# Kernel tuning notes

Hardware: AMD Instinct MI355X
Metric: run time of the kernel (lower is better)

## Reference

```python
import jax, jax.numpy as jnp
import numpy as np
from jax.scipy.special import gammaln

B, N, K = 16, 65536, 64


def setup_inputs() -> dict:
    key = jax.random.key(0)
    k1, k2, k3, k4, k5 = jax.random.split(key, 5)
    x = jax.random.normal(k1, (B, N), dtype=jnp.float32)
    loc = jnp.full((1,), 0.5, dtype=jnp.float32)          # mean of Normal alpha prior
    scale = jnp.full((1,), -2.0, dtype=jnp.float32)       # softplus(-2) ~ 0.127
    epsilon = jax.random.normal(k3, (1,), dtype=jnp.float32)
    lags = jax.random.randint(k4, (K,), 1, N - 1, dtype=jnp.int64)
    return {"x": x, "loc": loc, "scale": scale, "epsilon": epsilon, "lags": lags}


def _stochastic_frac_deriv(x, alpha, lags):
    """Monte-Carlo Marchaud fractional derivative with k sampled memory lags.

    D^a f(t) ~ a/Gamma(1-a) * (N-1)/k * sum_m (f(t) - f(t - j_m)) * j_m^{-a-1}
    with the term masked out when t < j_m (history does not exist).
    """
    n = x.shape[-1]
    k = lags.shape[0]
    j = jnp.clip(lags, 1, n - 1)                      # [k]
    t = jnp.arange(n)                                 # [N]
    idx = jnp.maximum(t[None, :] - j[:, None], 0)     # [k, N]
    mask = (t[None, :] >= j[:, None]).astype(x.dtype) # [k, N]
    w = j.astype(x.dtype) ** (-(alpha + 1.0))         # kernel weight s^{-a-1}, [k]
    c = alpha * jnp.exp(-gammaln(1.0 - alpha)) * (n - 1) / k  # normalization * MC volume
    xg = x[:, idx]                                    # [B, k, N] gathered history
    contrib = (x[:, None, :] - xg) * (mask * w[:, None])[None, :, :]
    return c * contrib.sum(axis=1)                    # [B, N]


def reference(x, loc, scale, epsilon, lags):
    # reparameterized alpha ~ Normal(loc, softplus(scale))
    alpha = (loc + jax.nn.softplus(scale) * epsilon)[0]
    alpha = jnp.clip(alpha, 0.01, 0.99)               # keep fractional order valid
    return _stochastic_frac_deriv(x, alpha, lags)
```

## Files before the change

kernel.cpp:

```cpp
#include <hip/hip_runtime.h>

#define BB 16
#define NN 65536
#define KK 64
#define TPB 256
#define CHUNK 512
#define NBLK ((BB * NN) / CHUNK)

__device__ __forceinline__ float readlane_f(float v, int lane) {
    return __uint_as_float((unsigned)__builtin_amdgcn_readlane((int)__float_as_uint(v), lane));
}

__global__ __launch_bounds__(TPB) void frac_deriv_kernel(
    const float* __restrict__ x,
    const float* __restrict__ loc,
    const float* __restrict__ scale,
    const float* __restrict__ eps,
    const int* __restrict__ lags,
    float* __restrict__ out)
{
    __shared__ int   js_raw[KK];
    __shared__ float ws_raw[KK];
    __shared__ int   js[KK];
    __shared__ float ws[KK];
    __shared__ int   cnt[2];

    const int tid = threadIdx.x;
    const int bid = blockIdx.x;
    const int swz = (bid & 7) * (NBLK / 8) + (bid >> 3);
    const int b   = swz >> 7;
    const int q   = swz & 127;
    const int T   = q * CHUNK;

    if (tid < KK) {
        double s  = (double)scale[0];
        double sp = (s > 20.0) ? s : log1p(exp(s));
        double a  = (double)loc[0] + sp * (double)eps[0];
        a = fmin(fmax(a, 0.01), 0.99);
        double c = a * exp(-lgamma(1.0 - a)) * ((double)(NN - 1) / (double)KK);
        int j = lags[tid];
        j = (j < 1) ? 1 : ((j > NN - 1) ? NN - 1 : j);
        js_raw[tid] = j;
        ws_raw[tid] = (float)(c * exp(-(a + 1.0) * log((double)j)));
    }
    __syncthreads();
    if (tid < KK) {
        const int j = js_raw[tid];
        int rank = 0;
        for (int k = 0; k < KK; ++k) {
            const int jk = js_raw[k];
            rank += (int)((jk < j) || (jk == j && k < tid));
        }
        js[rank] = j;
        ws[rank] = ws_raw[tid];
    }
    __syncthreads();
    if (tid < 64) {
        const int j = js[tid];
        const unsigned long long mf = __ballot(j <= T);
        const unsigned long long mp = __ballot(j <= T + (CHUNK - 1));
        if (tid == 0) { cnt[0] = __popcll(mf); cnt[1] = __popcll(mp); }
    }
    __syncthreads();

    const int   jv = js[tid & 63];
    const float wv = ws[tid & 63];

    const float* __restrict__ xr = x + (size_t)b * NN;
    const float xt0 = xr[T + tid];
    const float xt1 = xr[T + 256 + tid];

    double acc0 = 0.0, acc1 = 0.0;

    const int cf  = __builtin_amdgcn_readfirstlane(cnt[0]);
    const int cp  = __builtin_amdgcn_readfirstlane(cnt[1]);
    const int cf8 = cf & ~7;

    for (int mo = 0; mo < cf8; mo += 8) {
        float g0 = 0.0f, g1 = 0.0f;
#pragma unroll
        for (int mi = 0; mi < 8; ++mi) {
            const int   m  = mo + mi;
            const int   jj = __builtin_amdgcn_readlane(jv, m);
            const float w  = readlane_f(wv, m);
            const float* bp = xr + (T - jj);
            const float x0 = bp[tid];
            const float x1 = bp[tid + 256];
            g0 = fmaf(xt0 - x0, w, g0);
            g1 = fmaf(xt1 - x1, w, g1);
        }
        acc0 += (double)g0;
        acc1 += (double)g1;
    }
    for (int m = cf8; m < cf; ++m) {
        const int   jj = __builtin_amdgcn_readlane(jv, m);
        const float w  = readlane_f(wv, m);
        const float* bp = xr + (T - jj);
        acc0 += (double)((xt0 - bp[tid]) * w);
        acc1 += (double)((xt1 - bp[tid + 256]) * w);
    }
    for (int m = cf; m < cp; ++m) {
        const int   jj = __builtin_amdgcn_readlane(jv, m);
        const float w  = readlane_f(wv, m);
        const int d0 = T + tid - jj;
        const int d1 = d0 + 256;
        const float g0v = xr[(d0 < 0) ? 0 : d0];
        const float g1v = xr[(d1 < 0) ? 0 : d1];
        acc0 += (d0 >= 0) ? (double)((xt0 - g0v) * w) : 0.0;
        acc1 += (d1 >= 0) ? (double)((xt1 - g1v) * w) : 0.0;
    }

    float* __restrict__ orow = out + (size_t)b * NN;
    orow[T + tid]       = (float)acc0;
    orow[T + 256 + tid] = (float)acc1;
}

extern "C" void kernel_launch(void* const* d_in, const int* in_sizes, int n_in,
                              void* d_out, int out_size, void* d_ws, size_t ws_size,
                              hipStream_t stream) {
    const float* x     = (const float*)d_in[0];
    const float* loc   = (const float*)d_in[1];
    const float* scale = (const float*)d_in[2];
    const float* eps   = (const float*)d_in[3];
    const int*   lags  = (const int*)d_in[4];
    float* out = (float*)d_out;

    frac_deriv_kernel<<<NBLK, TPB, 0, stream>>>(x, loc, scale, eps, lags, out);
}
```

Measured before the change: 17.23 us.

## Hoist lag/weight setup into separate kernel; unroll gather loop by 16

Moves the per-block double-precision alpha/lgamma/weight computation and the lag sort into a one-block setup kernel that writes sorted lags and weights to workspace. The main kernel then reads them directly, computes the ballot counts per wave, and drops three block barriers and the shared arrays. The inner gather loop is unrolled to 16 with two independent accumulator chains, and block order is reversed so heavier chunks (high T) start first. This adds a second kernel launch and a dependency between the two kernels.

```diff
diff --git a/kernel.cpp b/kernel.cpp
--- a/kernel.cpp
+++ b/kernel.cpp
@@ -11,88 +11,82 @@
     return __uint_as_float((unsigned)__builtin_amdgcn_readlane((int)__float_as_uint(v), lane));
 }
 
+__global__ __launch_bounds__(KK) void setup_kernel(
+    const float* __restrict__ loc, const float* __restrict__ scale,
+    const float* __restrict__ eps, const int* __restrict__ lags,
+    int* __restrict__ js_out, float* __restrict__ ws_out)
+{
+    __shared__ int   jraw[KK];
+    __shared__ float wraw[KK];
+    const int tid = threadIdx.x;
+
+    double s  = (double)scale[0];
+    double sp = (s > 20.0) ? s : log1p(exp(s));
+    double a  = (double)loc[0] + sp * (double)eps[0];
+    a = fmin(fmax(a, 0.01), 0.99);
+    double c = a * exp(-lgamma(1.0 - a)) * ((double)(NN - 1) / (double)KK);
+
+    int j = lags[tid];
+    j = (j < 1) ? 1 : ((j > NN - 1) ? NN - 1 : j);
+    jraw[tid] = j;
+    wraw[tid] = (float)(c * exp(-(a + 1.0) * log((double)j)));
+    __syncthreads();
+
+    int rank = 0;
+    for (int k = 0; k < KK; ++k) {
+        const int jk = jraw[k];
+        rank += (int)((jk < j) || (jk == j && k < tid));
+    }
+    js_out[rank] = j;
+    ws_out[rank] = wraw[tid];
+}
+
 __global__ __launch_bounds__(TPB) void frac_deriv_kernel(
     const float* __restrict__ x,
-    const float* __restrict__ loc,
-    const float* __restrict__ scale,
-    const float* __restrict__ eps,
-    const int* __restrict__ lags,
+    const int* __restrict__ js,
+    const float* __restrict__ ws,
     float* __restrict__ out)
 {
-    __shared__ int   js_raw[KK];
-    __shared__ float ws_raw[KK];
-    __shared__ int   js[KK];
-    __shared__ float ws[KK];
-    __shared__ int   cnt[2];
-
     const int tid = threadIdx.x;
     const int bid = blockIdx.x;
     const int swz = (bid & 7) * (NBLK / 8) + (bid >> 3);
     const int b   = swz >> 7;
-    const int q   = swz & 127;
+    const int q   = 127 - (swz & 127);
     const int T   = q * CHUNK;
 
-    if (tid < KK) {
-        double s  = (double)scale[0];
-        double sp = (s > 20.0) ? s : log1p(exp(s));
-        double a  = (double)loc[0] + sp * (double)eps[0];
-        a = fmin(fmax(a, 0.01), 0.99);
-        double c = a * exp(-lgamma(1.0 - a)) * ((double)(NN - 1) / (double)KK);
-        int j = lags[tid];
-        j = (j < 1) ? 1 : ((j > NN - 1) ? NN - 1 : j);
-        js_raw[tid] = j;
-        ws_raw[tid] = (float)(c * exp(-(a + 1.0) * log((double)j)));
-    }
-    __syncthreads();
-    if (tid < KK) {
-        const int j = js_raw[tid];
-        int rank = 0;
-        for (int k = 0; k < KK; ++k) {
-            const int jk = js_raw[k];
-            rank += (int)((jk < j) || (jk == j && k < tid));
-        }
-        js[rank] = j;
-        ws[rank] = ws_raw[tid];
-    }
-    __syncthreads();
-    if (tid < 64) {
-        const int j = js[tid];
-        const unsigned long long mf = __ballot(j <= T);
-        const unsigned long long mp = __ballot(j <= T + (CHUNK - 1));
-        if (tid == 0) { cnt[0] = __popcll(mf); cnt[1] = __popcll(mp); }
-    }
-    __syncthreads();
-
-    const int   jv = js[tid & 63];
-    const float wv = ws[tid & 63];
+    const int   lane = tid & 63;
+    const int   jv   = js[lane];
+    const float wv   = ws[lane];
+    const int cf = __popcll(__ballot(jv <= T));
+    const int cp = __popcll(__ballot(jv <= T + (CHUNK - 1)));
 
     const float* __restrict__ xr = x + (size_t)b * NN;
     const float xt0 = xr[T + tid];
     const float xt1 = xr[T + 256 + tid];
 
     double acc0 = 0.0, acc1 = 0.0;
+    const int cf16 = cf & ~15;
 
-    const int cf  = __builtin_amdgcn_readfirstlane(cnt[0]);
-    const int cp  = __builtin_amdgcn_readfirstlane(cnt[1]);
-    const int cf8 = cf & ~7;
-
-    for (int mo = 0; mo < cf8; mo += 8) {
-        float g0 = 0.0f, g1 = 0.0f;
+    for (int mo = 0; mo < cf16; mo += 16) {
+        float g0a = 0.0f, g0b = 0.0f, g1a = 0.0f, g1b = 0.0f;
 #pragma unroll
-        for (int mi = 0; mi < 8; ++mi) {
-            const int   m  = mo + mi;
-            const int   jj = __builtin_amdgcn_readlane(jv, m);
-            const float w  = readlane_f(wv, m);
-            const float* bp = xr + (T - jj);
-            const float x0 = bp[tid];
-            const float x1 = bp[tid + 256];
-            g0 = fmaf(xt0 - x0, w, g0);
-            g1 = fmaf(xt1 - x1, w, g1);
+        for (int mi = 0; mi < 16; mi += 2) {
+            const int   m0 = mo + mi, m1 = mo + mi + 1;
+            const int   ja = __builtin_amdgcn_readlane(jv, m0);
+            const float wa = readlane_f(wv, m0);
+            const int   jb = __builtin_amdgcn_readlane(jv, m1);
+            const float wb = readlane_f(wv, m1);
+            const float* pa = xr + (T - ja);
+            const float* pb = xr + (T - jb);
+            g0a = fmaf(xt0 - pa[tid],       wa, g0a);
+            g1a = fmaf(xt1 - pa[tid + 256], wa, g1a);
+            g0b = fmaf(xt0 - pb[tid],       wb, g0b);
+            g1b = fmaf(xt1 - pb[tid + 256], wb, g1b);
         }
-        acc0 += (double)g0;
-        acc1 += (double)g1;
+        acc0 += (double)(g0a + g0b);
+        acc1 += (double)(g1a + g1b);
     }
-    for (int m = cf8; m < cf; ++m) {
+    for (int m = cf16; m < cf; ++m) {
         const int   jj = __builtin_amdgcn_readlane(jv, m);
         const float w  = readlane_f(wv, m);
         const float* bp = xr + (T - jj);
@@ -125,5 +119,9 @@
     const int*   lags  = (const int*)d_in[4];
     float* out = (float*)d_out;
 
-    frac_deriv_kernel<<<NBLK, TPB, 0, stream>>>(x, loc, scale, eps, lags, out);
+    int*   js_ws = (int*)d_ws;
+    float* ws_ws = (float*)((char*)d_ws + 256);
+
+    setup_kernel<<<1, KK, 0, stream>>>(loc, scale, eps, lags, js_ws, ws_ws);
+    frac_deriv_kernel<<<NBLK, TPB, 0, stream>>>(x, js_ws, ws_ws, out);
 }
```

Measured after the change: 18.29 us. 6.2% more time.

## Compute sorted lags per wavefront with cross-lane ops, drop LDS and barriers

Applied to the files above, without the earlier changes.

Each wavefront now computes alpha, the lag weights and the rank sort itself, using readlane and ds_permute instead of shared memory and three block barriers. Chunk-start counts come from a per-wave ballot. The main loop is unrolled to 16 and all gathered loads are issued before the FMAs to raise memory-level parallelism. Chunk order is reversed so blocks with more valid lags are scheduled first. In exchange, every wave redundantly evaluates the double-precision transcendental setup, and the unrolled loop uses more registers.

```diff
diff --git a/kernel.cpp b/kernel.cpp
--- a/kernel.cpp
+++ b/kernel.cpp
@@ -19,95 +19,74 @@
     const int* __restrict__ lags,
     float* __restrict__ out)
 {
-    __shared__ int   js_raw[KK];
-    __shared__ float ws_raw[KK];
-    __shared__ int   js[KK];
-    __shared__ float ws[KK];
-    __shared__ int   cnt[2];
+    const int tid  = threadIdx.x;
+    const int lane = tid & 63;
 
-    const int tid = threadIdx.x;
     const int bid = blockIdx.x;
     const int swz = (bid & 7) * (NBLK / 8) + (bid >> 3);
     const int b   = swz >> 7;
-    const int q   = swz & 127;
+    const int q   = 127 - (swz & 127);
     const int T   = q * CHUNK;
-
-    if (tid < KK) {
-        double s  = (double)scale[0];
-        double sp = (s > 20.0) ? s : log1p(exp(s));
-        double a  = (double)loc[0] + sp * (double)eps[0];
-        a = fmin(fmax(a, 0.01), 0.99);
-        double c = a * exp(-lgamma(1.0 - a)) * ((double)(NN - 1) / (double)KK);
-        int j = lags[tid];
-        j = (j < 1) ? 1 : ((j > NN - 1) ? NN - 1 : j);
-        js_raw[tid] = j;
-        ws_raw[tid] = (float)(c * exp(-(a + 1.0) * log((double)j)));
-    }
-    __syncthreads();
-    if (tid < KK) {
-        const int j = js_raw[tid];
-        int rank = 0;
-        for (int k = 0; k < KK; ++k) {
-            const int jk = js_raw[k];
-            rank += (int)((jk < j) || (jk == j && k < tid));
-        }
-        js[rank] = j;
-        ws[rank] = ws_raw[tid];
-    }
-    __syncthreads();
-    if (tid < 64) {
-        const int j = js[tid];
-        const unsigned long long mf = __ballot(j <= T);
-        const unsigned long long mp = __ballot(j <= T + (CHUNK - 1));
-        if (tid == 0) { cnt[0] = __popcll(mf); cnt[1] = __popcll(mp); }
-    }
-    __syncthreads();
-
-    const int   jv = js[tid & 63];
-    const float wv = ws[tid & 63];
 
     const float* __restrict__ xr = x + (size_t)b * NN;
     const float xt0 = xr[T + tid];
     const float xt1 = xr[T + 256 + tid];
 
+    double s  = (double)scale[0];
+    double sp = (s > 20.0) ? s : log1p(exp(s));
+    double a  = (double)loc[0] + sp * (double)eps[0];
+    a = fmin(fmax(a, 0.01), 0.99);
+    const double c = a * exp(-lgamma(1.0 - a)) * ((double)(NN - 1) / (double)KK);
+
+    int j = lags[lane];
+    j = (j < 1) ? 1 : ((j > NN - 1) ? NN - 1 : j);
+    const float w = (float)(c * exp(-(a + 1.0) * log((double)j)));
+
+    int rank = 0;
+#pragma unroll 8
+    for (int k = 0; k < KK; ++k) {
+        const int jk = __builtin_amdgcn_readlane(j, k);
+        rank += (int)((jk < j) || (jk == j && k < lane));
+    }
+    const int   jv = __builtin_amdgcn_ds_permute(rank << 2, j);
+    const float wv = __uint_as_float(
+        (unsigned)__builtin_amdgcn_ds_permute(rank << 2, (int)__float_as_uint(w)));
+
+    const int cf = __popcll(__ballot(jv <= T));
+    const int cp = __popcll(__ballot(jv <= T + (CHUNK - 1)));
+    const int cf16 = cf & ~15;
+
     double acc0 = 0.0, acc1 = 0.0;
 
-    const int cf  = __builtin_amdgcn_readfirstlane(cnt[0]);
-    const int cp  = __builtin_amdgcn_readfirstlane(cnt[1]);
-    const int cf8 = cf & ~7;
-
-    for (int mo = 0; mo < cf8; mo += 8) {
+    for (int mo = 0; mo < cf16; mo += 16) {
+        float v0[16], v1[16];
+#pragma unroll
+        for (int mi = 0; mi < 16; ++mi) {
+            const int jj = __builtin_amdgcn_readlane(jv, mo + mi);
+            const float* bp = xr + (T - jj);
+            v0[mi] = bp[tid];
+            v1[mi] = bp[tid + 256];
+        }
         float g0 = 0.0f, g1 = 0.0f;
 #pragma unroll
-        for (int mi = 0; mi < 8; ++mi) {
-            const int   m  = mo + mi;
-            const int   jj = __builtin_amdgcn_readlane(jv, m);
-            const float w  = readlane_f(wv, m);
-            const float* bp = xr + (T - jj);
-            const float x0 = bp[tid];
-            const float x1 = bp[tid + 256];
-            g0 = fmaf(xt0 - x0, w, g0);
-            g1 = fmaf(xt1 - x1, w, g1);
+        for (int mi = 0; mi < 16; ++mi) {
+            const float wm = readlane_f(wv, mo + mi);
+            g0 = fmaf(xt0 - v0[mi], wm, g0);
+            g1 = fmaf(xt1 - v1[mi], wm, g1);
         }
         acc0 += (double)g0;
         acc1 += (double)g1;
     }
-    for (int m = cf8; m < cf; ++m) {
+
+    for (int m = cf16; m < cp; ++m) {
         const int   jj = __builtin_amdgcn_readlane(jv, m);
-        const float w  = readlane_f(wv, m);
-        const float* bp = xr + (T - jj);
-        acc0 += (double)((xt0 - bp[tid]) * w);
-        acc1 += (double)((xt1 - bp[tid + 256]) * w);
-    }
-    for (int m = cf; m < cp; ++m) {
-        const int   jj = __builtin_amdgcn_readlane(jv, m);
-        const float w  = readlane_f(wv, m);
+        const float wm = readlane_f(wv, m);
         const int d0 = T + tid - jj;
         const int d1 = d0 + 256;
         const float g0v = xr[(d0 < 0) ? 0 : d0];
         const float g1v = xr[(d1 < 0) ? 0 : d1];
-        acc0 += (d0 >= 0) ? (double)((xt0 - g0v) * w) : 0.0;
-        acc1 += (d1 >= 0) ? (double)((xt1 - g1v) * w) : 0.0;
+        acc0 += (d0 >= 0) ? (double)((xt0 - g0v) * wm) : 0.0;
+        acc1 += (d1 >= 0) ? (double)((xt1 - g1v) * wm) : 0.0;
     }
 
     float* __restrict__ orow = out + (size_t)b * NN;
```

After: 27.36 us. 58.8% more time.

## Process four contiguous elements per thread with vector loads and 1024-element blocks

Applied to the files above, without the earlier changes.

Each thread now handles four contiguous outputs through 16-byte vector loads and stores, and each block covers 1024 elements instead of 512, halving the grid. The lag-count ballot now runs per wavefront, which removes one shared-memory round trip and a block barrier. The x-value load is issued before the alpha/weight setup so its latency overlaps that work. Gather loads shifted by arbitrary lags are often misaligned for float4, so the vector loads may split, and the block count drops, which reduces parallelism and latency hiding.

```diff
diff --git a/kernel.cpp b/kernel.cpp
--- a/kernel.cpp
+++ b/kernel.cpp
@@ -4,11 +4,17 @@
 #define NN 65536
 #define KK 64
 #define TPB 256
-#define CHUNK 512
-#define NBLK ((BB * NN) / CHUNK)
+#define EPB 1024
+#define NBLK ((BB * NN) / EPB)
 
 __device__ __forceinline__ float readlane_f(float v, int lane) {
     return __uint_as_float((unsigned)__builtin_amdgcn_readlane((int)__float_as_uint(v), lane));
+}
+
+__device__ __forceinline__ float4 load4(const float* p) {
+    float4 v;
+    __builtin_memcpy(&v, p, 16);
+    return v;
 }
 
 __global__ __launch_bounds__(TPB) void frac_deriv_kernel(
@@ -23,14 +29,19 @@
     __shared__ float ws_raw[KK];
     __shared__ int   js[KK];
     __shared__ float ws[KK];
-    __shared__ int   cnt[2];
 
-    const int tid = threadIdx.x;
+    const int tid  = threadIdx.x;
+    const int lane = tid & 63;
+
     const int bid = blockIdx.x;
     const int swz = (bid & 7) * (NBLK / 8) + (bid >> 3);
-    const int b   = swz >> 7;
-    const int q   = swz & 127;
-    const int T   = q * CHUNK;
+    const int b   = swz >> 6;
+    const int q   = swz & 63;
+    const int T   = q * EPB;
+
+    const float* __restrict__ xr = x + (size_t)b * NN;
+    const int e0 = T + 4 * tid;
+    const float4 xt = load4(xr + e0);
 
     if (tid < KK) {
         double s  = (double)scale[0];
@@ -55,64 +66,55 @@
         ws[rank] = ws_raw[tid];
     }
     __syncthreads();
-    if (tid < 64) {
-        const int j = js[tid];
-        const unsigned long long mf = __ballot(j <= T);
-        const unsigned long long mp = __ballot(j <= T + (CHUNK - 1));
-        if (tid == 0) { cnt[0] = __popcll(mf); cnt[1] = __popcll(mp); }
-    }
-    __syncthreads();
 
-    const int   jv = js[tid & 63];
-    const float wv = ws[tid & 63];
-
-    const float* __restrict__ xr = x + (size_t)b * NN;
-    const float xt0 = xr[T + tid];
-    const float xt1 = xr[T + 256 + tid];
-
-    double acc0 = 0.0, acc1 = 0.0;
-
-    const int cf  = __builtin_amdgcn_readfirstlane(cnt[0]);
-    const int cp  = __builtin_amdgcn_readfirstlane(cnt[1]);
+    const int   jv = js[lane];
+    const float wv = ws[lane];
+    const int cf = __popcll(__ballot(jv <= T));
+    const int cp = __popcll(__ballot(jv <= T + (EPB - 1)));
     const int cf8 = cf & ~7;
 
+    double a0 = 0.0, a1 = 0.0, a2 = 0.0, a3 = 0.0;
+
     for (int mo = 0; mo < cf8; mo += 8) {
-        float g0 = 0.0f, g1 = 0.0f;
+        float4 g = make_float4(0.f, 0.f, 0.f, 0.f);
 #pragma unroll
         for (int mi = 0; mi < 8; ++mi) {
             const int   m  = mo + mi;
             const int   jj = __builtin_amdgcn_readlane(jv, m);
             const float w  = readlane_f(wv, m);
-            const float* bp = xr + (T - jj);
-            const float x0 = bp[tid];
-            const float x1 = bp[tid + 256];
-            g0 = fmaf(xt0 - x0, w, g0);
-            g1 = fmaf(xt1 - x1, w, g1);
+            const float4 xg = load4(xr + (e0 - jj));
+            g.x = fmaf(xt.x - xg.x, w, g.x);
+            g.y = fmaf(xt.y - xg.y, w, g.y);
+            g.z = fmaf(xt.z - xg.z, w, g.z);
+            g.w = fmaf(xt.w - xg.w, w, g.w);
         }
-        acc0 += (double)g0;
-        acc1 += (double)g1;
+        a0 += (double)g.x; a1 += (double)g.y; a2 += (double)g.z; a3 += (double)g.w;
     }
     for (int m = cf8; m < cf; ++m) {
         const int   jj = __builtin_amdgcn_readlane(jv, m);
         const float w  = readlane_f(wv, m);
-        const float* bp = xr + (T - jj);
-        acc0 += (double)((xt0 - bp[tid]) * w);
-        acc1 += (double)((xt1 - bp[tid + 256]) * w);
+        const float4 xg = load4(xr + (e0 - jj));
+        a0 += (double)((xt.x - xg.x) * w);
+        a1 += (double)((xt.y - xg.y) * w);
+        a2 += (double)((xt.z - xg.z) * w);
+        a3 += (double)((xt.w - xg.w) * w);
     }
     for (int m = cf; m < cp; ++m) {
         const int   jj = __builtin_amdgcn_readlane(jv, m);
         const float w  = readlane_f(wv, m);
-        const int d0 = T + tid - jj;
-        const int d1 = d0 + 256;
-        const float g0v = xr[(d0 < 0) ? 0 : d0];
-        const float g1v = xr[(d1 < 0) ? 0 : d1];
-        acc0 += (d0 >= 0) ? (double)((xt0 - g0v) * w) : 0.0;
-        acc1 += (d1 >= 0) ? (double)((xt1 - g1v) * w) : 0.0;
+        const int d0 = e0 - jj;
+        const float g0 = xr[(d0     < 0) ? 0 : d0];
+        const float g1 = xr[(d0 + 1 < 0) ? 0 : d0 + 1];
+        const float g2 = xr[(d0 + 2 < 0) ? 0 : d0 + 2];
+        const float g3 = xr[(d0 + 3 < 0) ? 0 : d0 + 3];
+        a0 += (d0     >= 0) ? (double)((xt.x - g0) * w) : 0.0;
+        a1 += (d0 + 1 >= 0) ? (double)((xt.y - g1) * w) : 0.0;
+        a2 += (d0 + 2 >= 0) ? (double)((xt.z - g2) * w) : 0.0;
+        a3 += (d0 + 3 >= 0) ? (double)((xt.w - g3) * w) : 0.0;
     }
 
-    float* __restrict__ orow = out + (size_t)b * NN;
-    orow[T + tid]       = (float)acc0;
-    orow[T + 256 + tid] = (float)acc1;
+    float4 r = make_float4((float)a0, (float)a1, (float)a2, (float)a3);
+    __builtin_memcpy(out + (size_t)b * NN + e0, &r, 16);
 }
 
 extern "C" void kernel_launch(void* const* d_in, const int* in_sizes, int n_in,
```

New measurement: 16.61 us. -3.6%, faster.
